# Performance work log

Measured on AMD Instinct MI355X. Metric: run time of the kernel, lower is better.

The kernel has to match this reference:

```python
import jax, jax.numpy as jnp
from jax import lax
import numpy as np

B, N, P, NB = 64, 16, 20, 30      # frames, boxes/frame, num_persons, num_behaviors
C, F, OUT, SR = 1024, 14, 3, 2    # fmap channels, fmap size, roi output, sampling ratio
EPS = 1e-5


def roi_align_one(fmap, boxes):
    """fmap: [C,H,W]; boxes: [K,4]=(x1,y1,x2,y2) in fmap coords. Returns [K,C,OUT,OUT].
    torchvision-style roi_align (aligned=False) with fixed sampling_ratio=SR."""
    H, W = fmap.shape[1], fmap.shape[2]
    x1, y1, x2, y2 = boxes[:, 0], boxes[:, 1], boxes[:, 2], boxes[:, 3]
    rw = jnp.maximum(x2 - x1, 1.0)
    rh = jnp.maximum(y2 - y1, 1.0)
    S = OUT * SR
    pos = (jnp.arange(S, dtype=fmap.dtype) + 0.5) / SR            # sample pos in bin units
    ys = jnp.clip(y1[:, None] + pos[None, :] * (rh / OUT)[:, None], 0.0, H - 1.0)  # [K,S]
    xs = jnp.clip(x1[:, None] + pos[None, :] * (rw / OUT)[:, None], 0.0, W - 1.0)
    y0 = jnp.floor(ys); x0 = jnp.floor(xs)
    y0i = y0.astype(jnp.int32); x0i = x0.astype(jnp.int32)
    y1i = jnp.minimum(y0i + 1, H - 1); x1i = jnp.minimum(x0i + 1, W - 1)
    wy = ys - y0; wx = xs - x0                                     # [K,S]
    g = lambda yi, xi: fmap[:, yi[:, :, None], xi[:, None, :]]     # [C,K,S,S]
    v = (g(y0i, x0i) * ((1 - wy)[:, :, None] * (1 - wx)[:, None, :])
         + g(y0i, x1i) * ((1 - wy)[:, :, None] * wx[:, None, :])
         + g(y1i, x0i) * (wy[:, :, None] * (1 - wx)[:, None, :])
         + g(y1i, x1i) * (wy[:, :, None] * wx[:, None, :]))
    v = jnp.transpose(v, (1, 0, 2, 3))                             # [K,C,S,S]
    K = boxes.shape[0]
    return v.reshape(K, C, OUT, SR, OUT, SR).mean(axis=(3, 5))     # avg over samples


roi_align = jax.vmap(roi_align_one, in_axes=(0, 0))


def bn(x, g, b, m, v):
    s = (g / jnp.sqrt(v + EPS))[None, :, None, None]
    return x * s + (b - m * g / jnp.sqrt(v + EPS))[None, :, None, None]


def leaky(x):
    return jnp.where(x > 0, x, 0.1 * x)


def behavior_conv(x, w1, g1, b1, m1, v1, w2, g2, b2, m2, v2):
    dn = ('NCHW', 'OIHW', 'NCHW')
    x = lax.conv_general_dilated(x, w1, (1, 1), 'SAME', dimension_numbers=dn)
    x = leaky(bn(x, g1, b1, m1, v1))
    x = lax.conv_general_dilated(x, w2, (1, 1), 'SAME', dimension_numbers=dn)
    return leaky(bn(x, g2, b2, m2, v2))


def forward(fmap, boxes, conv1_w, bn1_g, bn1_b, bn1_m, bn1_v,
            conv2_w, bn2_g, bn2_b, bn2_m, bn2_v,
            conv1d_w, conv1d_b, fc1_w, fc1_b, fc2_w, fc2_b, person_idx):
    # --- global feature: ROI over the whole fmap per frame ---
    gbox = jnp.broadcast_to(jnp.array([[0.0, 0.0, F, F]], jnp.float32), (B, 1, 4))
    g_roi = roi_align(fmap, gbox).reshape(B, C, OUT, OUT)          # [B,1024,3,3]
    g_feat = behavior_conv(g_roi, conv1_w, bn1_g, bn1_b, bn1_m, bn1_v,
                           conv2_w, bn2_g, bn2_b, bn2_m, bn2_v)    # [B,256,3,3]
    g_feat = g_feat.reshape(B, 256 * OUT * OUT)                    # [B,2304]

    # --- per-box ROI features ---
    i_roi = roi_align(fmap, boxes).reshape(B * N, C, OUT, OUT)     # [B*N,1024,3,3]
    i_feat = behavior_conv(i_roi, conv1_w, bn1_g, bn1_b, bn1_m, bn1_v,
                           conv2_w, bn2_g, bn2_b, bn2_m, bn2_v)
    i_feat = i_feat.reshape(B, N, 256 * OUT * OUT)                 # [B,N,2304]

    # --- scatter-accumulate into behavior tensor [B,P,2304] ---
    behavior = jnp.broadcast_to(g_feat[:, None, :], (B, P, 2304))
    bidx = jnp.broadcast_to(jnp.arange(B)[:, None], (B, N))
    behavior = behavior.at[bidx, person_idx].add(i_feat)

    # --- temporal conv1d across the batch axis for every person slot ---
    x = jnp.transpose(behavior, (1, 2, 0))                         # [P,2304,B]
    x = lax.conv_general_dilated(x, conv1d_w, (1,), 'SAME',
                                 dimension_numbers=('NCH', 'OIH', 'NCH'))
    x = x + conv1d_b[None, :, None]                                # [P,2304,B]

    # --- gather each (frame, box)'s person feature at its frame and classify ---
    x = jnp.transpose(x, (2, 0, 1))                                # [B,P,2304]
    feats = jnp.take_along_axis(x, person_idx[:, :, None], axis=1) # [B,N,2304]
    h = jax.nn.relu(feats @ fc1_w + fc1_b)                         # dropout off (eval)
    return h @ fc2_w + fc2_b                                       # [B,N,NB]


def setup_inputs() -> dict:
    key = jax.random.key(0)
    ks = jax.random.split(key, 16)
    fmap = jax.random.normal(ks[0], (B, C, F, F), jnp.float32)
    lo = jax.random.uniform(ks[1], (B, N, 2), jnp.float32, 0.0, 9.0)
    sz = jax.random.uniform(ks[2], (B, N, 2), jnp.float32, 2.0, 5.0)
    hi = jnp.minimum(lo + sz, float(F))
    boxes = jnp.concatenate([lo, hi], axis=-1)                     # (x1,y1,x2,y2)
    person_idx = jax.random.randint(ks[3], (B, N), 0, P)
    s = lambda k, shape, fan: jax.random.normal(k, shape, jnp.float32) / np.sqrt(fan)
    return {
        'fmap': fmap, 'boxes': boxes, 'person_idx': person_idx,
        'conv1_w': s(ks[4], (512, 1024, 3, 3), 1024 * 9),
        'bn1_g': jnp.ones(512), 'bn1_b': jnp.zeros(512),
        'bn1_m': jnp.zeros(512), 'bn1_v': jnp.ones(512),
        'conv2_w': s(ks[5], (256, 512, 3, 3), 512 * 9),
        'bn2_g': jnp.ones(256), 'bn2_b': jnp.zeros(256),
        'bn2_m': jnp.zeros(256), 'bn2_v': jnp.ones(256),
        'conv1d_w': s(ks[6], (2304, 2304, 3), 2304 * 3),
        'conv1d_b': jnp.zeros(2304),
        'fc1_w': s(ks[7], (2304, 1024), 2304), 'fc1_b': jnp.zeros(1024),
        'fc2_w': s(ks[8], (1024, NB), 1024), 'fc2_b': jnp.zeros(NB),
    }


def reference(fmap, boxes, person_idx, conv1_w, bn1_g, bn1_b, bn1_m, bn1_v,
              conv2_w, bn2_g, bn2_b, bn2_m, bn2_v,
              conv1d_w, conv1d_b, fc1_w, fc1_b, fc2_w, fc2_b):
    return forward(fmap, boxes, conv1_w, bn1_g, bn1_b, bn1_m, bn1_v,
                   conv2_w, bn2_g, bn2_b, bn2_m, bn2_v,
                   conv1d_w, conv1d_b, fc1_w, fc1_b, fc2_w, fc2_b, person_idx)
```

## Files before the change

kernel.cpp:

```cpp
#include <hip/hip_runtime.h>
#include <hip/hip_bf16.h>
#include <cstdint>
#include <cstddef>

typedef __bf16 bf16;
typedef __bf16 bf16x8 __attribute__((ext_vector_type(8)));
typedef float f32x4 __attribute__((ext_vector_type(4)));

__device__ __forceinline__ void gload_lds16(const bf16* g, bf16* l) {
    __builtin_amdgcn_global_load_lds((const __attribute__((address_space(1))) void*)g,
                                     (__attribute__((address_space(3))) void*)l, 16, 0, 0);
}

__device__ __forceinline__ int block_tap_mask(int y) {
    int lo = (y * 128) / 1088;
    int hiRow = y * 128 + 127; if (hiRow > 9791) hiRow = 9791;
    int hi = hiRow / 1088;
    int msk = 0;
    for (int pos = lo; pos <= hi; ++pos) {
        int oy = pos / 3, ox = pos - oy * 3;
        int ym = oy == 0 ? 6 : (oy == 1 ? 7 : 3);
        int xm = ox == 0 ? 6 : (ox == 1 ? 7 : 3);
        #pragma unroll
        for (int ty = 0; ty < 3; ty++)
            #pragma unroll
            for (int tx = 0; tx < 3; tx++)
                if (((ym >> ty) & 1) & ((xm >> tx) & 1))
                    msk |= 1 << (ty * 3 + tx);
    }
    return msk;
}

template <int NT>
__global__ void __launch_bounds__(256) repack_w(const float* __restrict__ w, bf16* __restrict__ out,
                                                int OC, int IC) {
    int idx = blockIdx.x * 256 + threadIdx.x;
    if (idx >= OC * IC) return;
    int oc = idx / IC;
    int ic = idx - oc * IC;
    const float* src = w + (size_t)idx * NT;
    #pragma unroll
    for (int t = 0; t < NT; t++)
        out[(size_t)oc * NT * IC + t * IC + ic] = (bf16)src[t];
}

__global__ void __launch_bounds__(256) repack_w9_both(const float* __restrict__ wa, bf16* __restrict__ oa,
                                                      const float* __restrict__ wb, bf16* __restrict__ ob) {
    int idx = blockIdx.x * 256 + threadIdx.x;
    if (idx < 512 * 1024) {
        int oc = idx >> 10, ic = idx & 1023;
        const float* src = wa + (size_t)idx * 9;
        #pragma unroll
        for (int t = 0; t < 9; t++)
            oa[(size_t)oc * 9216 + t * 1024 + ic] = (bf16)src[t];
    } else {
        int k = idx - 512 * 1024;
        if (k < 256 * 512) {
            int oc = k >> 9, ic = k & 511;
            const float* src = wb + (size_t)k * 9;
            #pragma unroll
            for (int t = 0; t < 9; t++)
                ob[(size_t)oc * 4608 + t * 512 + ic] = (bf16)src[t];
        }
    }
}

__global__ void __launch_bounds__(256) transpose_fc1(const float* __restrict__ w, bf16* __restrict__ out) {
    __shared__ float t[32][33];
    int iT = blockIdx.x * 32;
    int oT = blockIdx.y * 32;
    int tx = threadIdx.x, ty = threadIdx.y;
    #pragma unroll
    for (int j = 0; j < 4; j++)
        t[ty + j * 8][tx] = w[(size_t)(iT + ty + j * 8) * 1024 + oT + tx];
    __syncthreads();
    #pragma unroll
    for (int j = 0; j < 4; j++)
        out[(size_t)(oT + ty + j * 8) * 2304 + iT + tx] = (bf16)t[tx][ty + j * 8];
}

__global__ void __launch_bounds__(256) setup_all(int* __restrict__ rb1t, int* __restrict__ rb2t,
                                                 int* __restrict__ rb1dg, int* __restrict__ rbid,
                                                 int* __restrict__ tapmask,
                                                 int* __restrict__ tasks1, int* __restrict__ tasks2,
                                                 const int* __restrict__ pidx,
                                                 bf16* __restrict__ zp1, bf16* __restrict__ zp2,
                                                 bf16* __restrict__ zp3,
                                                 const float* g1, const float* b1, const float* m1, const float* v1,
                                                 const float* g2, const float* b2, const float* m2, const float* v2,
                                                 float* __restrict__ s1, float* __restrict__ t1,
                                                 float* __restrict__ s2, float* __restrict__ t2,
                                                 const float* __restrict__ fc2_w, bf16* __restrict__ w2t) {
    int m = blockIdx.x * 256 + threadIdx.x;
    if (m < 9 * 9856) {
        int tap = m / 9856, r = m - tap * 9856;
        int mm = r < 9792 ? r : 0;
        int pos = mm / 1088, img = mm - pos * 1088;
        int oy = pos / 3, ox = pos - oy * 3;
        int ty = tap / 3, tx = tap - ty * 3;
        int iy = oy + ty - 1, ix = ox + tx - 1;
        bool valid = (iy >= 0) & (iy < 3) & (ix >= 0) & (ix < 3);
        int cell = iy * 3 + ix;
        rb1t[m] = valid ? 1024 + (img * 9 + cell) * 1024 : 0;
        rb2t[m] = valid ? 512 + (cell * 1088 + img) * 512 : 0;
    }
    if (m < 77) tapmask[m] = block_tap_mask(m);
    if (blockIdx.x == 0) {
        __shared__ int sT[77], sB1[78], sB2[78];
        __shared__ int e1y[164], e1j[164], e1w[164];
        __shared__ int e2y[130], e2j[130], e2w[130];
        int t = threadIdx.x;
        if (t < 77) sT[t] = __popc(block_tap_mask(t));
        __syncthreads();
        if (t == 0) {
            int a1 = 0, a2 = 0;
            for (int y = 0; y < 77; ++y) {
                sB1[y] = a1; a1 += (sT[y] + 2) / 3;
                sB2[y] = a2; a2 += (sT[y] + 3) / 4;
            }
            sB1[77] = a1;
            sB2[77] = a2;
        }
        __syncthreads();
        if (t < 77) {
            int T = sT[t];
            int J1 = (T + 2) / 3, J2 = (T + 3) / 4;
            int w1[3] = {0, 0, 0}, w2[3] = {0, 0, 0};
            for (int o = 0; o < T; ++o) { w1[o * J1 / T]++; w2[o * J2 / T]++; }
            for (int jj = 0; jj < J1; ++jj) {
                int e = sB1[t] + jj;
                e1y[e] = t; e1j[e] = jj; e1w[e] = w1[jj];
            }
            for (int jj = 0; jj < J2; ++jj) {
                int e = sB2[t] + jj;
                e2y[e] = t; e2j[e] = jj; e2w[e] = w2[jj];
            }
        }
        __syncthreads();
        if (t < 164) {
            int wv = e1w[t], rank = 0;
            for (int e2i = 0; e2i < 164; ++e2i)
                rank += (e1w[e2i] > wv) | ((e1w[e2i] == wv) & (e2i < t));
            int pk = (e1y[t] << 5) | (e1j[t] << 2);
            #pragma unroll
            for (int nt = 0; nt < 4; ++nt) {
                int idx = (rank < 160) ? ((rank & 7) + (((rank >> 3) * 4 + nt) << 3))
                                       : (640 + (rank - 160) * 4 + nt);
                tasks1[idx] = pk | nt;
            }
        }
        if (t < 130) {
            int wv = e2w[t], rank = 0;
            for (int e2i = 0; e2i < 130; ++e2i)
                rank += (e2w[e2i] > wv) | ((e2w[e2i] == wv) & (e2i < t));
            int pk = (e2y[t] << 5) | (e2j[t] << 2);
            #pragma unroll
            for (int nt = 0; nt < 2; ++nt) {
                int idx = (rank < 128) ? ((rank & 7) + (((rank >> 3) * 2 + nt) << 3))
                                       : (256 + (rank - 128) * 2 + nt);
                tasks2[idx] = pk | nt;
            }
        }
    }
    if (m < 3 * 1024) {
        int tap = m / 1024, r = m - tap * 1024;
        int b = r >> 4;
        int p = pidx[r];
        int tt = b + tap - 1;
        bool valid = (tt >= 0) & (tt < 64);
        rb1dg[m] = valid ? 2304 + (p * 64 + tt) * 2304 : 0;
    }
    if (m < 1024) rbid[m] = m * 2304;
    if (m < 30 * 1024) {
        int n = m / 1024, k = m - n * 1024;
        w2t[m] = (bf16)fc2_w[(size_t)k * 30 + n];
    }
    if (m < 1024) zp1[m] = (bf16)0.f;
    if (m < 512)  zp2[m] = (bf16)0.f;
    if (m < 2304) zp3[m] = (bf16)0.f;
    if (m < 512) {
        float sc = g1[m] * rsqrtf(v1[m] + 1e-5f);
        s1[m] = sc; t1[m] = b1[m] - m1[m] * sc;
    } else if (m < 768) {
        int i = m - 512;
        float sc = g2[i] * rsqrtf(v2[i] + 1e-5f);
        s2[i] = sc; t2[i] = b2[i] - m2[i] * sc;
    }
}

__global__ void __launch_bounds__(256) transpose_fmap(const float* __restrict__ fmap, bf16* __restrict__ fml) {
    __shared__ float t[32][33];
    int img = blockIdx.z;
    int hwT = blockIdx.x * 32;
    int cT  = blockIdx.y * 32;
    int tx = threadIdx.x, ty = threadIdx.y;
    #pragma unroll
    for (int j = 0; j < 4; j++) {
        int c = cT + ty + j * 8;
        int hw = hwT + tx;
        if (hw < 196)
            t[ty + j * 8][tx] = fmap[((size_t)img * 1024 + c) * 196 + hw];
    }
    __syncthreads();
    #pragma unroll
    for (int j = 0; j < 4; j++) {
        int hw = hwT + ty + j * 8;
        int c = cT + tx;
        if (hw < 196)
            fml[((size_t)img * 196 + hw) * 1024 + c] = (bf16)t[tx][ty + j * 8];
    }
}

__global__ void __launch_bounds__(128) roi_kernel2(const bf16* __restrict__ fml, const float* __restrict__ boxes,
                                                   bf16* __restrict__ a1c) {
    int box = blockIdx.x;
    int tid = threadIdx.x;
    float x1, y1, x2, y2;
    int img;
    if (box < 64) { img = box; x1 = 0.f; y1 = 0.f; x2 = 14.f; y2 = 14.f; }
    else {
        int ib = box - 64;
        img = ib >> 4;
        const float* bb = boxes + (size_t)ib * 4;
        x1 = bb[0]; y1 = bb[1]; x2 = bb[2]; y2 = bb[3];
    }
    float rw = fmaxf(x2 - x1, 1.f), rh = fmaxf(y2 - y1, 1.f);
    __shared__ float swy[6], swx[6];
    __shared__ int sy0[6], sx0[6];
    if (tid < 6) {
        int i = tid;
        float pos = ((float)i + 0.5f) * 0.5f;
        float yv = fminf(fmaxf(y1 + pos * (rh * (1.f / 3.f)), 0.f), 13.f);
        float y0 = floorf(yv);
        sy0[i] = (int)y0; swy[i] = yv - y0;
        float xv = fminf(fmaxf(x1 + pos * (rw * (1.f / 3.f)), 0.f), 13.f);
        float x0 = floorf(xv);
        sx0[i] = (int)x0; swx[i] = xv - x0;
    }
    __syncthreads();
    const bf16* base = fml + (size_t)img * 196 * 1024 + tid * 8;
    #pragma unroll
    for (int oy = 0; oy < 3; oy++) {
        #pragma unroll
        for (int ox = 0; ox < 3; ox++) {
            float acc[8];
            #pragma unroll
            for (int e = 0; e < 8; e++) acc[e] = 0.f;
            #pragma unroll
            for (int dy = 0; dy < 2; dy++) {
                int sy = 2 * oy + dy;
                int y0 = sy0[sy]; float wy = swy[sy];
                int y1i = min(y0 + 1, 13);
                #pragma unroll
                for (int dx = 0; dx < 2; dx++) {
                    int sx = 2 * ox + dx;
                    int x0 = sx0[sx]; float wx = swx[sx];
                    int x1i = min(x0 + 1, 13);
                    bf16x8 f00 = *(const bf16x8*)(base + (size_t)(y0 * 14 + x0) * 1024);
                    bf16x8 f01 = *(const bf16x8*)(base + (size_t)(y0 * 14 + x1i) * 1024);
                    bf16x8 f10 = *(const bf16x8*)(base + (size_t)(y1i * 14 + x0) * 1024);
                    bf16x8 f11 = *(const bf16x8*)(base + (size_t)(y1i * 14 + x1i) * 1024);
                    float w00 = (1.f - wy) * (1.f - wx), w01 = (1.f - wy) * wx;
                    float w10 = wy * (1.f - wx),         w11 = wy * wx;
                    #pragma unroll
                    for (int e = 0; e < 8; e++)
                        acc[e] += w00 * (float)f00[e] + w01 * (float)f01[e]
                                + w10 * (float)f10[e] + w11 * (float)f11[e];
                }
            }
            bf16x8 o;
            #pragma unroll
            for (int e = 0; e < 8; e++) o[e] = (bf16)(acc[e] * 0.25f);
            *(bf16x8*)(a1c + 1024 + ((size_t)box * 9 + oy * 3 + ox) * 1024 + tid * 8) = o;
        }
    }
}

__global__ void __launch_bounds__(256) assemble(const float* __restrict__ feat, const int* __restrict__ pidx,
                                                bf16* __restrict__ asm3) {
    int b = blockIdx.x;
    int p = blockIdx.y;
    __shared__ int idxs[16];
    if (threadIdx.x < 16) idxs[threadIdx.x] = pidx[b * 16 + threadIdx.x];
    __syncthreads();
    const float* g = feat + (size_t)b * 2304;
    for (int f = threadIdx.x; f < 2304; f += 256) {
        float v = g[f];
        #pragma unroll
        for (int n = 0; n < 16; n++)
            if (idxs[n] == p) v += feat[(size_t)(64 + b * 16 + n) * 2304 + f];
        asm3[2304 + ((size_t)p * 64 + b) * 2304 + f] = (bf16)v;
    }
}

template <int MODE, int NSPLIT>
__global__ void __launch_bounds__(256) gemm_k(const bf16* __restrict__ A, const int* __restrict__ rowtab,
                                              const bf16* __restrict__ Bw, float* __restrict__ outp,
                                              const int* __restrict__ tapmask,
                                              const int* __restrict__ tasklist) {
    constexpr int K   = MODE == 0 ? 9216 : MODE == 1 ? 4608 : MODE == 2 ? 6912 : 2304;
    constexpr int N   = MODE == 0 ? 512  : MODE == 1 ? 256  : MODE == 2 ? 2304 : 1024;
    constexpr int Cin = MODE == 0 ? 1024 : MODE == 1 ? 512  : 2304;
    constexpr int M   = MODE <= 1 ? 9792 : 1024;
    constexpr int MT  = MODE <= 1 ? 9856 : 1024;
    constexpr bool MPAD = (M % 128) != 0;
    constexpr int KTS = (K / 64) / NSPLIT;

    const int tid = threadIdx.x;
    const int lane = tid & 63, wave = tid >> 6;
    const int q = lane >> 4, ln16 = lane & 15;
    const int wr = wave >> 1, wc = wave & 1;

    __shared__ __align__(16) bf16 As[128 * 64];
    __shared__ __align__(16) bf16 Bs[128 * 64];

    const int sr = lane >> 3;
    const int sc = ((lane & 7) ^ sr) * 8;

    int bm, bn, z;
    int mask = 0, T = 0, J = 0, jsel = 0;
    if constexpr (MODE <= 1) {
        const int pk = tasklist[blockIdx.x];
        const int y = pk >> 5;
        jsel = (pk >> 2) & 7;
        const int nt = pk & 3;
        bm = y * 128; bn = nt * 128; z = jsel;
        mask = tapmask[y];
        T = __popc(mask);
        J = MODE == 0 ? (T + 2) / 3 : (T + 3) / 4;
    } else {
        bm = blockIdx.y * 128;
        bn = blockIdx.x * 128;
        z = blockIdx.z;
    }

    const bf16* gB[4];
    #pragma unroll
    for (int u = 0; u < 4; u++)
        gB[u] = Bw + (size_t)(bn + wave * 32 + u * 8 + sr) * K + sc;

    f32x4 acc[4][4];
    #pragma unroll
    for (int mt = 0; mt < 4; mt++)
        #pragma unroll
        for (int nn = 0; nn < 4; nn++)
            acc[mt][nn] = (f32x4){0.f, 0.f, 0.f, 0.f};

    if constexpr (MODE <= 1) {
        int ord = 0;
        for (int tap = 0; tap < 9; ++tap) {
            if (!((mask >> tap) & 1)) continue;
            const int o = ord++;
            if (o * J / T != jsel) continue;
            int rbA[4];
            #pragma unroll
            for (int u = 0; u < 4; u++)
                rbA[u] = rowtab[tap * MT + bm + wave * 32 + u * 8 + sr];
            for (int kk = 0; kk < Cin / 64; ++kk) {
                const int aoff = kk * 64 + sc;
                const int k0 = tap * Cin + kk * 64;

                __syncthreads();
                #pragma unroll
                for (int u = 0; u < 4; u++)
                    gload_lds16(A + (size_t)(rbA[u] + aoff), As + (wave * 32 + u * 8) * 64);
                #pragma unroll
                for (int u = 0; u < 4; u++)
                    gload_lds16(gB[u] + k0, Bs + (wave * 32 + u * 8) * 64);
                __syncthreads();

                #pragma unroll
                for (int s = 0; s < 2; s++) {
                    bf16x8 af[4], bfr[4];
                    #pragma unroll
                    for (int mt = 0; mt < 4; mt++) {
                        int r = wr * 64 + mt * 16 + ln16;
                        af[mt] = *(const bf16x8*)(As + r * 64 + (((4 * s + q) ^ (ln16 & 7)) << 3));
                    }
                    #pragma unroll
                    for (int nn = 0; nn < 4; nn++) {
                        int r = wc * 64 + nn * 16 + ln16;
                        bfr[nn] = *(const bf16x8*)(Bs + r * 64 + (((4 * s + q) ^ (ln16 & 7)) << 3));
                    }
                    #pragma unroll
                    for (int mt = 0; mt < 4; mt++)
                        #pragma unroll
                        for (int nn = 0; nn < 4; nn++)
                            acc[mt][nn] = __builtin_amdgcn_mfma_f32_16x16x32_bf16(af[mt], bfr[nn], acc[mt][nn], 0, 0, 0);
                }
            }
        }
    } else {
        int rbA[4];
        int curtap = -1;
        for (int kt = z * KTS; kt < z * KTS + KTS; kt++) {
            const int k0 = kt * 64;
            const int tap = k0 / Cin;
            const int inner = k0 - tap * Cin;
            if (tap != curtap) {
                curtap = tap;
                #pragma unroll
                for (int u = 0; u < 4; u++)
                    rbA[u] = rowtab[tap * MT + bm + wave * 32 + u * 8 + sr];
            }
            const int aoff = inner + sc;

            __syncthreads();
            #pragma unroll
            for (int u = 0; u < 4; u++)
                gload_lds16(A + (size_t)(rbA[u] + aoff), As + (wave * 32 + u * 8) * 64);
            #pragma unroll
            for (int u = 0; u < 4; u++)
                gload_lds16(gB[u] + k0, Bs + (wave * 32 + u * 8) * 64);
            __syncthreads();

            #pragma unroll
            for (int s = 0; s < 2; s++) {
                bf16x8 af[4], bfr[4];
                #pragma unroll
                for (int mt = 0; mt < 4; mt++) {
                    int r = wr * 64 + mt * 16 + ln16;
                    af[mt] = *(const bf16x8*)(As + r * 64 + (((4 * s + q) ^ (ln16 & 7)) << 3));
                }
                #pragma unroll
                for (int nn = 0; nn < 4; nn++) {
                    int r = wc * 64 + nn * 16 + ln16;
                    bfr[nn] = *(const bf16x8*)(Bs + r * 64 + (((4 * s + q) ^ (ln16 & 7)) << 3));
                }
                #pragma unroll
                for (int mt = 0; mt < 4; mt++)
                    #pragma unroll
                    for (int nn = 0; nn < 4; nn++)
                        acc[mt][nn] = __builtin_amdgcn_mfma_f32_16x16x32_bf16(af[mt], bfr[nn], acc[mt][nn], 0, 0, 0);
            }
        }
    }

    #pragma unroll
    for (int mt = 0; mt < 4; mt++) {
        int gmBase = bm + wr * 64 + mt * 16 + q * 4;
        #pragma unroll
        for (int r = 0; r < 4; r++) {
            int gm = gmBase + r;
            if (MPAD && gm >= M) continue;
            #pragma unroll
            for (int nn = 0; nn < 4; nn++) {
                int gn = bn + wc * 64 + nn * 16 + ln16;
                outp[((size_t)z * M + gm) * N + gn] = acc[mt][nn][r];
            }
        }
    }
}

__global__ void __launch_bounds__(256) reduce0_tiled(const float* __restrict__ part,
                                                     float* __restrict__ feat,
                                                     const float* __restrict__ s2, const float* __restrict__ t2,
                                                     const int* __restrict__ tapm) {
    int c = blockIdx.x;
    int t = threadIdx.x;
    float acc[9];
    #pragma unroll
    for (int r = 0; r < 9; r++) {
        int m = r * 1088 + c;
        int y = m >> 7;
        int J = (__popc(tapm[y]) + 3) / 4;
        const float* p0 = part + (size_t)m * 256 + t;
        float v = p0[0];
        if (J >= 2) v += p0[(size_t)9792 * 256];
        if (J >= 3) v += p0[(size_t)2 * 9792 * 256];
        acc[r] = v;
    }
    float s = s2[t], b = t2[t];
    __shared__ float L[9 * 257];
    #pragma unroll
    for (int r = 0; r < 9; r++) {
        float v = acc[r] * s + b;
        v = v > 0.f ? v : 0.1f * v;
        L[r * 257 + t] = v;
    }
    __syncthreads();
    float* fout = feat + (size_t)c * 2304;
    #pragma unroll
    for (int k = 0; k < 9; k++) {
        int f = t + k * 256;
        int oc = f / 9, pos = f - oc * 9;
        fout[f] = L[pos * 257 + oc];
    }
}

template <int RMODE>
__global__ void __launch_bounds__(256) reduce_k(const float* __restrict__ part, void* __restrict__ outp,
                                                const float* __restrict__ c0, const float* __restrict__ c1,
                                                const int* __restrict__ tapm) {
    constexpr int M = RMODE == 1 ? 1024 : RMODE == 2 ? 1024 : 9792;
    constexpr int N = RMODE == 1 ? 2304 : RMODE == 2 ? 1024 : 512;
    constexpr int S = RMODE == 1 ? 3    : RMODE == 2 ? 4    : 2;
    int idx = blockIdx.x * 256 + threadIdx.x;
    if (idx >= M * N) return;
    int m = idx / N, n = idx - m * N;
    float v = 0.f;
    #pragma unroll
    for (int s = 0; s < S; s++) v += part[(size_t)s * M * N + idx];
    if constexpr (RMODE == 1) {
        v += c0[n];
        ((bf16*)outp)[idx] = (bf16)v;
    } else if constexpr (RMODE == 2) {
        v = fmaxf(v + c0[n], 0.f);
        ((bf16*)outp)[idx] = (bf16)v;
    } else {
        int y = m >> 7;
        int J = (__popc(tapm[y]) + 2) / 3;
        if (J == 3) v += part[(size_t)2 * M * N + idx];
        v = v * c0[n] + c1[n];
        v = v > 0.f ? v : 0.1f * v;
        ((bf16*)outp)[512 + (size_t)m * 512 + n] = (bf16)v;
    }
}

__global__ void __launch_bounds__(256) fc2_kernel(const bf16* __restrict__ h, const bf16* __restrict__ w2t,
                                                  const float* __restrict__ b2, float* __restrict__ out) {
    int tid = threadIdx.x;
    int m = blockIdx.x * 8 + (tid >> 5);
    int n = tid & 31;
    int n2 = n < 30 ? n : 29;
    const bf16* hr = h + (size_t)m * 1024;
    const bf16* wr = w2t + (size_t)n2 * 1024;
    float acc = 0.f;
    for (int k = 0; k < 1024; k += 8) {
        bf16x8 hv = *(const bf16x8*)(hr + k);
        bf16x8 wv = *(const bf16x8*)(wr + k);
        #pragma unroll
        for (int e = 0; e < 8; e++) acc += (float)hv[e] * (float)wv[e];
    }
    if (n < 30) out[(size_t)m * 30 + n] = acc + b2[n];
}

extern "C" void kernel_launch(void* const* d_in, const int* in_sizes, int n_in,
                              void* d_out, int out_size, void* d_ws, size_t ws_size,
                              hipStream_t stream) {
    const float* fmap     = (const float*)d_in[0];
    const float* boxes    = (const float*)d_in[1];
    const int*   pidx     = (const int*)d_in[2];
    const float* conv1_w  = (const float*)d_in[3];
    const float* bn1_g    = (const float*)d_in[4];
    const float* bn1_b    = (const float*)d_in[5];
    const float* bn1_m    = (const float*)d_in[6];
    const float* bn1_v    = (const float*)d_in[7];
    const float* conv2_w  = (const float*)d_in[8];
    const float* bn2_g    = (const float*)d_in[9];
    const float* bn2_b    = (const float*)d_in[10];
    const float* bn2_m    = (const float*)d_in[11];
    const float* bn2_v    = (const float*)d_in[12];
    const float* conv1d_w = (const float*)d_in[13];
    const float* conv1d_b = (const float*)d_in[14];
    const float* fc1_w    = (const float*)d_in[15];
    const float* fc1_b    = (const float*)d_in[16];
    const float* fc2_w    = (const float*)d_in[17];
    const float* fc2_b    = (const float*)d_in[18];
    float* out = (float*)d_out;

    char* ws = (char*)d_ws;

    float* s1    = (float*)(ws + 0);
    float* t1    = (float*)(ws + 2048);
    float* s2    = (float*)(ws + 4096);
    float* t2    = (float*)(ws + 5120);
    int*   rbid  = (int*)(ws + 6144);
    int*   rb1dg = (int*)(ws + 10240);
    int*   tapm  = (int*)(ws + 22528);
    int*   rb1t  = (int*)(ws + 25600);
    int*   rb2t  = (int*)(ws + 380416);
    int*   tasks1 = (int*)(ws + 735232);
    int*   tasks2 = (int*)(ws + 738944);
    bf16*  fml    = (bf16*)(ws + 768000);
    float* part1  = (float*)(ws + 768000);
    float* part2  = (float*)(ws + 768000);
    float* part1d = (float*)(ws + 768000);
    float* partfc = (float*)(ws + 768000);
    bf16*  a1c    = (bf16*)(ws + 60930048);
    bf16*  wb1d   = (bf16*)(ws + 60930048);
    bf16*  fc1t   = (bf16*)(ws + 92780544);
    bf16*  xbuf   = (bf16*)(ws + 97499136);
    bf16*  hbuf   = (bf16*)(ws + 102217728);
    bf16*  w2t    = (bf16*)(ws + 104314880);
    bf16*  wb1    = (bf16*)(ws + 104857600);
    bf16*  wb2    = (bf16*)(ws + 114294784);
    bf16*  a2c    = (bf16*)(ws + 116654080);
    bf16*  asm3   = (bf16*)(ws + 126682112);
    float* feat   = (float*)(ws + 132584960);

    bf16* zp1 = a1c;
    bf16* zp2 = a2c;
    bf16* zp3 = asm3;

    setup_all<<<(9 * 9856 + 255) / 256, 256, 0, stream>>>(rb1t, rb2t, rb1dg, rbid, tapm,
                                                          tasks1, tasks2, pidx,
                                                          zp1, zp2, zp3,
                                                          bn1_g, bn1_b, bn1_m, bn1_v,
                                                          bn2_g, bn2_b, bn2_m, bn2_v,
                                                          s1, t1, s2, t2, fc2_w, w2t);
    repack_w9_both<<<2560, 256, 0, stream>>>(conv1_w, wb1, conv2_w, wb2);

    transpose_fmap<<<dim3(7, 32, 64), dim3(32, 8), 0, stream>>>(fmap, fml);
    roi_kernel2<<<1088, 128, 0, stream>>>(fml, boxes, a1c);

    gemm_k<0, 3><<<656, 256, 0, stream>>>(a1c, rb1t, wb1, part1, tapm, tasks1);
    reduce_k<3><<<(9792 * 512 + 255) / 256, 256, 0, stream>>>(part1, a2c, s1, t1, tapm);

    repack_w<3><<<(2304 * 2304 + 255) / 256, 256, 0, stream>>>(conv1d_w, wb1d, 2304, 2304);
    transpose_fc1<<<dim3(72, 32), dim3(32, 8), 0, stream>>>(fc1_w, fc1t);

    gemm_k<1, 3><<<260, 256, 0, stream>>>(a2c, rb2t, wb2, part2, tapm, tasks2);
    reduce0_tiled<<<1088, 256, 0, stream>>>(part2, feat, s2, t2, tapm);
    assemble<<<dim3(64, 20), 256, 0, stream>>>(feat, pidx, asm3);
    gemm_k<2, 3><<<dim3(18, 8, 3), 256, 0, stream>>>(asm3, rb1dg, wb1d, part1d, tapm, nullptr);
    reduce_k<1><<<(1024 * 2304 + 255) / 256, 256, 0, stream>>>(part1d, xbuf, conv1d_b, nullptr, nullptr);
    gemm_k<3, 4><<<dim3(8, 8, 4), 256, 0, stream>>>(xbuf, rbid, fc1t, partfc, tapm, nullptr);
    reduce_k<2><<<(1024 * 1024 + 255) / 256, 256, 0, stream>>>(partfc, hbuf, fc1_b, nullptr, nullptr);
    fc2_kernel<<<128, 256, 0, stream>>>(hbuf, w2t, fc2_b, out);
    (void)in_sizes; (void)n_in; (void)out_size; (void)ws_size;
}
```

Measured before the change: 465.0 us.

## Fuse fc1 split-K reduction into fc2 and rebalance conv2 task split

Two changes. The fc1 split-K reduce plus ReLU is merged into the fc2 kernel: each block sums the four partials for one row into shared memory and computes the 30 outputs there, so the bf16 hidden buffer and one launch go away. Conv2's tap-split task list now uses the same 3-taps-per-chunk split as conv1 (more chunks, 328 blocks instead of 260), giving more parallel blocks at the cost of more partial sums to write and reduce. The reduction in reduce0_tiled is adjusted to match.

```diff
diff --git a/kernel.cpp b/kernel.cpp
--- a/kernel.cpp
+++ b/kernel.cpp
@@ -106,34 +106,25 @@
     }
     if (m < 77) tapmask[m] = block_tap_mask(m);
     if (blockIdx.x == 0) {
-        __shared__ int sT[77], sB1[78], sB2[78];
+        __shared__ int sT[77], sB1[78];
         __shared__ int e1y[164], e1j[164], e1w[164];
-        __shared__ int e2y[130], e2j[130], e2w[130];
         int t = threadIdx.x;
         if (t < 77) sT[t] = __popc(block_tap_mask(t));
         __syncthreads();
         if (t == 0) {
-            int a1 = 0, a2 = 0;
-            for (int y = 0; y < 77; ++y) {
-                sB1[y] = a1; a1 += (sT[y] + 2) / 3;
-                sB2[y] = a2; a2 += (sT[y] + 3) / 4;
-            }
+            int a1 = 0;
+            for (int y = 0; y < 77; ++y) { sB1[y] = a1; a1 += (sT[y] + 2) / 3; }
             sB1[77] = a1;
-            sB2[77] = a2;
         }
         __syncthreads();
         if (t < 77) {
             int T = sT[t];
-            int J1 = (T + 2) / 3, J2 = (T + 3) / 4;
-            int w1[3] = {0, 0, 0}, w2[3] = {0, 0, 0};
-            for (int o = 0; o < T; ++o) { w1[o * J1 / T]++; w2[o * J2 / T]++; }
-            for (int jj = 0; jj < J1; ++jj) {
+            int J = (T + 2) / 3;
+            int w[3] = {0, 0, 0};
+            for (int o = 0; o < T; ++o) w[o * J / T]++;
+            for (int jj = 0; jj < J; ++jj) {
                 int e = sB1[t] + jj;
-                e1y[e] = t; e1j[e] = jj; e1w[e] = w1[jj];
-            }
-            for (int jj = 0; jj < J2; ++jj) {
-                int e = sB2[t] + jj;
-                e2y[e] = t; e2j[e] = jj; e2w[e] = w2[jj];
+                e1y[e] = t; e1j[e] = jj; e1w[e] = w[jj];
             }
         }
         __syncthreads();
@@ -148,16 +139,10 @@
                                        : (640 + (rank - 160) * 4 + nt);
                 tasks1[idx] = pk | nt;
             }
-        }
-        if (t < 130) {
-            int wv = e2w[t], rank = 0;
-            for (int e2i = 0; e2i < 130; ++e2i)
-                rank += (e2w[e2i] > wv) | ((e2w[e2i] == wv) & (e2i < t));
-            int pk = (e2y[t] << 5) | (e2j[t] << 2);
             #pragma unroll
             for (int nt = 0; nt < 2; ++nt) {
-                int idx = (rank < 128) ? ((rank & 7) + (((rank >> 3) * 2 + nt) << 3))
-                                       : (256 + (rank - 128) * 2 + nt);
+                int idx = (rank < 160) ? ((rank & 7) + (((rank >> 3) * 2 + nt) << 3))
+                                       : (320 + (rank - 160) * 2 + nt);
                 tasks2[idx] = pk | nt;
             }
         }
@@ -327,7 +312,7 @@
         bm = y * 128; bn = nt * 128; z = jsel;
         mask = tapmask[y];
         T = __popc(mask);
-        J = MODE == 0 ? (T + 2) / 3 : (T + 3) / 4;
+        J = (T + 2) / 3;
     } else {
         bm = blockIdx.y * 128;
         bn = blockIdx.x * 128;
@@ -463,11 +448,10 @@
     for (int r = 0; r < 9; r++) {
         int m = r * 1088 + c;
         int y = m >> 7;
-        int J = (__popc(tapm[y]) + 3) / 4;
+        int J = (__popc(tapm[y]) + 2) / 3;
         const float* p0 = part + (size_t)m * 256 + t;
-        float v = p0[0];
-        if (J >= 2) v += p0[(size_t)9792 * 256];
-        if (J >= 3) v += p0[(size_t)2 * 9792 * 256];
+        float v = p0[0] + p0[(size_t)9792 * 256];
+        if (J == 3) v += p0[(size_t)2 * 9792 * 256];
         acc[r] = v;
     }
     float s = s2[t], b = t2[t];
@@ -492,9 +476,9 @@
 __global__ void __launch_bounds__(256) reduce_k(const float* __restrict__ part, void* __restrict__ outp,
                                                 const float* __restrict__ c0, const float* __restrict__ c1,
                                                 const int* __restrict__ tapm) {
-    constexpr int M = RMODE == 1 ? 1024 : RMODE == 2 ? 1024 : 9792;
-    constexpr int N = RMODE == 1 ? 2304 : RMODE == 2 ? 1024 : 512;
-    constexpr int S = RMODE == 1 ? 3    : RMODE == 2 ? 4    : 2;
+    constexpr int M = RMODE == 1 ? 1024 : 9792;
+    constexpr int N = RMODE == 1 ? 2304 : 512;
+    constexpr int S = RMODE == 1 ? 3    : 2;
     int idx = blockIdx.x * 256 + threadIdx.x;
     if (idx >= M * N) return;
     int m = idx / N, n = idx - m * N;
@@ -503,9 +487,6 @@
     for (int s = 0; s < S; s++) v += part[(size_t)s * M * N + idx];
     if constexpr (RMODE == 1) {
         v += c0[n];
-        ((bf16*)outp)[idx] = (bf16)v;
-    } else if constexpr (RMODE == 2) {
-        v = fmaxf(v + c0[n], 0.f);
         ((bf16*)outp)[idx] = (bf16)v;
     } else {
         int y = m >> 7;
@@ -517,22 +498,42 @@
     }
 }
 
-__global__ void __launch_bounds__(256) fc2_kernel(const bf16* __restrict__ h, const bf16* __restrict__ w2t,
-                                                  const float* __restrict__ b2, float* __restrict__ out) {
-    int tid = threadIdx.x;
-    int m = blockIdx.x * 8 + (tid >> 5);
-    int n = tid & 31;
-    int n2 = n < 30 ? n : 29;
-    const bf16* hr = h + (size_t)m * 1024;
-    const bf16* wr = w2t + (size_t)n2 * 1024;
-    float acc = 0.f;
-    for (int k = 0; k < 1024; k += 8) {
-        bf16x8 hv = *(const bf16x8*)(hr + k);
-        bf16x8 wv = *(const bf16x8*)(wr + k);
-        #pragma unroll
-        for (int e = 0; e < 8; e++) acc += (float)hv[e] * (float)wv[e];
-    }
-    if (n < 30) out[(size_t)m * 30 + n] = acc + b2[n];
+__global__ void __launch_bounds__(256) fc1red_fc2(const float* __restrict__ part,
+                                                  const float* __restrict__ b1,
+                                                  const bf16* __restrict__ w2t,
+                                                  const float* __restrict__ b2,
+                                                  float* __restrict__ out) {
+    int m = blockIdx.x;
+    int t = threadIdx.x;
+    __shared__ float h[1024];
+    __shared__ float red[256];
+    #pragma unroll
+    for (int i = 0; i < 4; i++) {
+        int k = t + i * 256;
+        float v = 0.f;
+        #pragma unroll
+        for (int s = 0; s < 4; s++) v += part[((size_t)s * 1024 + m) * 1024 + k];
+        h[k] = fmaxf(v + b1[k], 0.f);
+    }
+    __syncthreads();
+    {
+        int c = t >> 5, n = t & 31;
+        float acc = 0.f;
+        if (n < 30) {
+            const bf16* wr = w2t + (size_t)n * 1024 + c * 128;
+            const float* hh = h + c * 128;
+            #pragma unroll
+            for (int k = 0; k < 128; k++) acc += hh[k] * (float)wr[k];
+        }
+        red[t] = acc;
+    }
+    __syncthreads();
+    if (t < 30) {
+        float acc = 0.f;
+        #pragma unroll
+        for (int c = 0; c < 8; c++) acc += red[c * 32 + t];
+        out[(size_t)m * 30 + t] = acc + b2[t];
+    }
 }
 
 extern "C" void kernel_launch(void* const* d_in, const int* in_sizes, int n_in,
@@ -581,7 +582,6 @@
     bf16*  wb1d   = (bf16*)(ws + 60930048);
     bf16*  fc1t   = (bf16*)(ws + 92780544);
     bf16*  xbuf   = (bf16*)(ws + 97499136);
-    bf16*  hbuf   = (bf16*)(ws + 102217728);
     bf16*  w2t    = (bf16*)(ws + 104314880);
     bf16*  wb1    = (bf16*)(ws + 104857600);
     bf16*  wb2    = (bf16*)(ws + 114294784);
@@ -610,13 +610,12 @@
     repack_w<3><<<(2304 * 2304 + 255) / 256, 256, 0, stream>>>(conv1d_w, wb1d, 2304, 2304);
     transpose_fc1<<<dim3(72, 32), dim3(32, 8), 0, stream>>>(fc1_w, fc1t);
 
-    gemm_k<1, 3><<<260, 256, 0, stream>>>(a2c, rb2t, wb2, part2, tapm, tasks2);
+    gemm_k<1, 3><<<328, 256, 0, stream>>>(a2c, rb2t, wb2, part2, tapm, tasks2);
     reduce0_tiled<<<1088, 256, 0, stream>>>(part2, feat, s2, t2, tapm);
     assemble<<<dim3(64, 20), 256, 0, stream>>>(feat, pidx, asm3);
     gemm_k<2, 3><<<dim3(18, 8, 3), 256, 0, stream>>>(asm3, rb1dg, wb1d, part1d, tapm, nullptr);
     reduce_k<1><<<(1024 * 2304 + 255) / 256, 256, 0, stream>>>(part1d, xbuf, conv1d_b, nullptr, nullptr);
     gemm_k<3, 4><<<dim3(8, 8, 4), 256, 0, stream>>>(xbuf, rbid, fc1t, partfc, tapm, nullptr);
-    reduce_k<2><<<(1024 * 1024 + 255) / 256, 256, 0, stream>>>(partfc, hbuf, fc1_b, nullptr, nullptr);
-    fc2_kernel<<<128, 256, 0, stream>>>(hbuf, w2t, fc2_b, out);
+    fc1red_fc2<<<1024, 256, 0, stream>>>(partfc, fc1_b, w2t, fc2_b, out);
     (void)in_sizes; (void)n_in; (void)out_size; (void)ws_size;
 }
```

Measured after the change: 446.0 us. 1.04x faster.
